# Performance work log

Hardware: AMD Instinct MI355X
Metric: run time of the kernel (lower is better)

The kernel has to match this reference:

```python
import jax, jax.numpy as jnp
import numpy as np

H = 16  # num_heads
B, N, M, D = 4, 512, 2048, 1024
FF = 4096  # mlp_ratio * D
LN_EPS = 1e-5


def _ln(x, g, b):
    m = x.mean(-1, keepdims=True)
    v = ((x - m) ** 2).mean(-1, keepdims=True)
    return (x - m) * jax.lax.rsqrt(v + LN_EPS) * g + b


def _attn(q_in, k_in, v_in, wq, bq, wk, bk, wv, bv, wp, bp):
    b, n, d = q_in.shape
    m = k_in.shape[1]
    hd = d // H
    scale = hd ** -0.5
    q = (q_in @ wq + bq).reshape(b, n, H, hd) * scale
    k = (k_in @ wk + bk).reshape(b, m, H, hd)
    v = (v_in @ wv + bv).reshape(b, m, H, hd)
    attn = jax.nn.softmax(jnp.einsum('bnhd,bmhd->bhnm', q, k), axis=-1)
    out = jnp.einsum('bhnm,bmhd->bnhd', attn, v).reshape(b, n, d)
    return out @ wp + bp


def setup_inputs() -> dict:
    key = jax.random.key(0)
    ks = iter(jax.random.split(key, 32))
    rnd = lambda shape: jax.random.normal(next(ks), shape, dtype=jnp.float32)
    w = lambda *shape: rnd(shape) * 0.02
    inp = {
        'state': rnd((B, N, D)),
        'patches': rnd((B, M, D)),
        'patches_pos_embed': rnd((B, M, D)),
        'state_query': rnd((B, N, D)),
    }
    for p in ('ca', 'sa'):
        inp[f'{p}_wq'] = w(D, D); inp[f'{p}_bq'] = jnp.zeros((D,), jnp.float32)
        inp[f'{p}_wk'] = w(D, D); inp[f'{p}_bk'] = jnp.zeros((D,), jnp.float32)
        inp[f'{p}_wv'] = w(D, D); inp[f'{p}_bv'] = jnp.zeros((D,), jnp.float32)
        inp[f'{p}_wp'] = w(D, D); inp[f'{p}_bp'] = jnp.zeros((D,), jnp.float32)
    inp['w1'] = w(D, FF); inp['b1'] = jnp.zeros((FF,), jnp.float32)
    inp['w2'] = w(FF, D); inp['b2'] = jnp.zeros((D,), jnp.float32)
    for i in (1, 2, 3):
        inp[f'n{i}_g'] = jnp.ones((D,), jnp.float32)
        inp[f'n{i}_b'] = jnp.zeros((D,), jnp.float32)
        inp[f'ls{i}'] = jnp.full((D,), 1e-5, jnp.float32)
    return inp


def reference(state, patches, patches_pos_embed, state_query,
              ca_wq, ca_bq, ca_wk, ca_bk, ca_wv, ca_bv, ca_wp, ca_bp,
              sa_wq, sa_bq, sa_wk, sa_bk, sa_wv, sa_bv, sa_wp, sa_bp,
              w1, b1, w2, b2,
              n1_g, n1_b, n2_g, n2_b, n3_g, n3_b,
              ls1, ls2, ls3):
    # pre-norm path of TransformerLayer.forward_pre (dropouts/drop_path = 0)
    state = state + state_query
    kv = patches + patches_pos_embed
    cross = _attn(_ln(state, n1_g, n1_b), kv, patches,
                  ca_wq, ca_bq, ca_wk, ca_bk, ca_wv, ca_bv, ca_wp, ca_bp)
    state = state + cross * ls1
    ns = _ln(state, n2_g, n2_b)
    selfa = _attn(ns, ns, ns,
                  sa_wq, sa_bq, sa_wk, sa_bk, sa_wv, sa_bv, sa_wp, sa_bp)
    state = state + selfa * ls2
    h = jax.nn.gelu(_ln(state, n3_g, n3_b) @ w1 + b1)
    return state + (h @ w2 + b2) * ls3
```

## Files before the change

### kernel.cpp

```cpp
#include <hip/hip_runtime.h>

#define DEV __device__ __forceinline__

typedef __bf16 bf16x8 __attribute__((ext_vector_type(8)));
typedef float f32x4 __attribute__((ext_vector_type(4)));

DEV unsigned short f2bf(float f) {
  __bf16 h = (__bf16)f;
  return __builtin_bit_cast(unsigned short, h);
}
DEV unsigned int cvtpk(float lo, float hi) {
  unsigned int r;
  asm("v_cvt_pk_bf16_f32 %0, %1, %2" : "=v"(r) : "v"(lo), "v"(hi));
  return r;
}

DEV void gload16(const void* g, void* l) {
  __builtin_amdgcn_global_load_lds(
      (const __attribute__((address_space(1))) unsigned int*)g,
      (__attribute__((address_space(3))) unsigned int*)l, 16, 0, 0);
}

DEV void tconv64_body(const float* __restrict__ W, unsigned short* __restrict__ Wt,
                      int K, int N, int bx, int by, float* tile ) {
  const int t = threadIdx.x;
  const int rr = t >> 4;
  const int cc = (t & 15) * 4;
#pragma unroll
  for (int it = 0; it < 4; it++) {
    float4 v = *reinterpret_cast<const float4*>(
        &W[(size_t)(by * 64 + it * 16 + rr) * N + bx * 64 + cc]);
    tile[(it * 16 + rr) * 65 + cc] = v.x;
    tile[(it * 16 + rr) * 65 + cc + 1] = v.y;
    tile[(it * 16 + rr) * 65 + cc + 2] = v.z;
    tile[(it * 16 + rr) * 65 + cc + 3] = v.w;
  }
  __syncthreads();
  const int nr = t >> 3;
  const int kc = (t & 7) * 8;
#pragma unroll
  for (int it = 0; it < 2; it++) {
    const int n = it * 32 + nr;
    uint4 o;
    o.x = cvtpk(tile[(kc + 0) * 65 + n], tile[(kc + 1) * 65 + n]);
    o.y = cvtpk(tile[(kc + 2) * 65 + n], tile[(kc + 3) * 65 + n]);
    o.z = cvtpk(tile[(kc + 4) * 65 + n], tile[(kc + 5) * 65 + n]);
    o.w = cvtpk(tile[(kc + 6) * 65 + n], tile[(kc + 7) * 65 + n]);
    *reinterpret_cast<uint4*>(&Wt[(size_t)(bx * 64 + n) * K + by * 64 + kc]) = o;
  }
}

DEV void add_ln_body(const float* __restrict__ a, const float* b, float* x0_out,
                     unsigned short* __restrict__ y, const float* __restrict__ gam,
                     const float* __restrict__ bet, int row) {
  const int t = threadIdx.x;
  const int c = t * 4;
  const size_t base = (size_t)row * 1024 + c;
  float4 v = *reinterpret_cast<const float4*>(a + base);
  if (b) {
    float4 v2 = *reinterpret_cast<const float4*>(b + base);
    v.x += v2.x; v.y += v2.y; v.z += v2.z; v.w += v2.w;
  }
  if (x0_out) *reinterpret_cast<float4*>(x0_out + base) = v;
  float s = v.x + v.y + v.z + v.w;
  float sq = v.x * v.x + v.y * v.y + v.z * v.z + v.w * v.w;
#pragma unroll
  for (int o = 32; o > 0; o >>= 1) {
    s += __shfl_xor(s, o);
    sq += __shfl_xor(sq, o);
  }
  __shared__ float ps[4], pq[4];
  const int w = t >> 6;
  if ((t & 63) == 0) { ps[w] = s; pq[w] = sq; }
  __syncthreads();
  s = ps[0] + ps[1] + ps[2] + ps[3];
  sq = pq[0] + pq[1] + pq[2] + pq[3];
  const float mean = s * (1.f / 1024.f);
  const float var = sq * (1.f / 1024.f) - mean * mean;
  const float rstd = rsqrtf(var + 1e-5f);
  float4 gv = *reinterpret_cast<const float4*>(gam + c);
  float4 bv = *reinterpret_cast<const float4*>(bet + c);
  uint2 o2;
  o2.x = cvtpk((v.x - mean) * rstd * gv.x + bv.x, (v.y - mean) * rstd * gv.y + bv.y);
  o2.y = cvtpk((v.z - mean) * rstd * gv.z + bv.z, (v.w - mean) * rstd * gv.w + bv.w);
  *reinterpret_cast<uint2*>(y + base) = o2;
}

DEV void kvcast_body8(const float* __restrict__ p, const float* __restrict__ pe,
                      unsigned short* __restrict__ kvo, unsigned short* __restrict__ po,
                      int bid) {
  const size_t i = ((size_t)bid * 256 + threadIdx.x) * 8;
  float4 a0 = *reinterpret_cast<const float4*>(p + i);
  float4 a1 = *reinterpret_cast<const float4*>(p + i + 4);
  float4 b0 = *reinterpret_cast<const float4*>(pe + i);
  float4 b1 = *reinterpret_cast<const float4*>(pe + i + 4);
  uint4 kv, pp;
  kv.x = cvtpk(a0.x + b0.x, a0.y + b0.y);
  kv.y = cvtpk(a0.z + b0.z, a0.w + b0.w);
  kv.z = cvtpk(a1.x + b1.x, a1.y + b1.y);
  kv.w = cvtpk(a1.z + b1.z, a1.w + b1.w);
  pp.x = cvtpk(a0.x, a0.y);
  pp.y = cvtpk(a0.z, a0.w);
  pp.z = cvtpk(a1.x, a1.y);
  pp.w = cvtpk(a1.z, a1.w);
  *reinterpret_cast<uint4*>(kvo + i) = kv;
  *reinterpret_cast<uint4*>(po + i) = pp;
}

struct Pre {
  const float* caw[3]; unsigned short* cad[3];
  const float* state; const float* squery; float* stateF; unsigned short* lnB;
  const float* n1_g; const float* n1_b;
  const float* patches; const float* ppe; unsigned short* kvB; unsigned short* patB;
};
__global__ __launch_bounds__(256) void prelude_kernel(Pre p) {
  __shared__ __align__(16) float tile[64 * 65];
  const int bid = blockIdx.x;
  if (bid < 4096) {
    kvcast_body8(p.patches, p.ppe, p.kvB, p.patB, bid);
  } else if (bid < 4864) {
    const int i = bid - 4096;
    const int m = i >> 8, wi = i & 255;
    tconv64_body(p.caw[m], p.cad[m], 1024, 1024, wi & 15, wi >> 4, tile);
  } else {
    add_ln_body(p.state, p.squery, p.stateF, p.lnB, p.n1_g, p.n1_b, bid - 4864);
  }
}

__global__ __launch_bounds__(256) void add_ln_kernel(
    const float* __restrict__ a, const float* b, float* x0_out,
    unsigned short* __restrict__ y, const float* __restrict__ gam,
    const float* __restrict__ bet) {
  add_ln_body(a, b, x0_out, y, gam, bet, blockIdx.x);
}

DEV void xcd_swizzle(int gx, int gy, int& bx, int& by, int& bz) {
  const int gxy = gx * gy;
  const int nwg = gxy * gridDim.z;
  const int orig = (blockIdx.z * gy + blockIdx.y) * gx + blockIdx.x;
  const int q = nwg >> 3, r = nwg & 7;
  const int xcd = orig & 7;
  int wgid = (xcd < r ? xcd * (q + 1) : r * (q + 1) + (xcd - r) * q) + (orig >> 3);
  bz = wgid / gxy;
  wgid -= bz * gxy;
  if (gy >= gx) { by = wgid / gx; bx = wgid - by * gx; }
  else          { bx = wgid / gy; by = wgid - bx * gy; }
}

template <int BM, int BN>
DEV void gemm_core(const unsigned short* __restrict__ A,
                   const unsigned short* __restrict__ Bt,
                   unsigned short* As, unsigned short* Bs,
                   int brow, int bcol, int K, int lda, int koff,
                   f32x4 (&acc)[BM / 32][BN / 32]) {
  constexpr int WM = BM / 32, WN = BN / 32;
  const int t = threadIdx.x;
  const int lane = t & 63, w = t >> 6;
  const int wr = w >> 1, wc = w & 1;
  const int g = lane >> 4, lr = lane & 15;
  const int srow = lane >> 2, scol = (lane & 3) * 8;

  auto stage = [&](int buf, int k0) {
#pragma unroll
    for (int i = 0; i < BM / 64; i++) {
      const int r0 = (i * 4 + w) * 16;
      gload16(A + (size_t)(brow + r0 + srow) * lda + koff + k0 + scol,
              &As[buf * BM * 32 + r0 * 32]);
    }
#pragma unroll
    for (int i = 0; i < BN / 64; i++) {
      const int r0 = (i * 4 + w) * 16;
      gload16(Bt + (size_t)(bcol + r0 + srow) * lda + koff + k0 + scol,
              &Bs[buf * BN * 32 + r0 * 32]);
    }
  };

  stage(0, 0);
  const int nk = K / 32;
  int cur = 0;
  for (int kt = 0; kt < nk; kt++) {
    __syncthreads();
    if (kt + 1 < nk) stage(cur ^ 1, (kt + 1) * 32);
    bf16x8 af[WM], bfr[WN];
#pragma unroll
    for (int m = 0; m < WM; m++)
      af[m] = *reinterpret_cast<const bf16x8*>(
          &As[cur * BM * 32 + (wr * (BM / 2) + m * 16 + lr) * 32 + g * 8]);
#pragma unroll
    for (int n = 0; n < WN; n++)
      bfr[n] = *reinterpret_cast<const bf16x8*>(
          &Bs[cur * BN * 32 + (wc * (BN / 2) + n * 16 + lr) * 32 + g * 8]);
    __builtin_amdgcn_s_setprio(1);
#pragma unroll
    for (int m = 0; m < WM; m++)
#pragma unroll
      for (int n = 0; n < WN; n++)
        acc[m][n] = __builtin_amdgcn_mfma_f32_16x16x32_bf16(af[m], bfr[n], acc[m][n], 0, 0, 0);
    __builtin_amdgcn_s_setprio(0);
    cur ^= 1;
  }
}

template <int BM, int BN>
DEV void epilogue_vT(f32x4 (&acc)[BM / 32][BN / 32], unsigned short* smem,
                     unsigned short* __restrict__ vT, const float* __restrict__ bias,
                     int brow, int bcol, int vcol0, int vNk, int rpb) {
  constexpr int WM = BM / 32, WN = BN / 32;
  constexpr int LDT = 136;
  const int t = threadIdx.x, lane = t & 63, w = t >> 6;
  const int wr = w >> 1, wc = w & 1;
  const int g = lane >> 4, lr = lane & 15;
  __syncthreads();
#pragma unroll
  for (int m = 0; m < WM; m++) {
    const int row0 = wr * (BM / 2) + m * 16 + g * 4;
#pragma unroll
    for (int n = 0; n < WN; n++) {
      const int cc = wc * (BN / 2) + n * 16 + lr;
      const float bv = bias[bcol + cc];
      uint2 pk;
      pk.x = cvtpk(acc[m][n][0] + bv, acc[m][n][1] + bv);
      pk.y = cvtpk(acc[m][n][2] + bv, acc[m][n][3] + bv);
      *reinterpret_cast<uint2*>(&smem[cc * LDT + row0]) = pk;
    }
  }
  __syncthreads();
  const int b = brow / rpb;
  const int kvb = brow % rpb;
  constexpr int ITERS = BM * BN / (256 * 8);
#pragma unroll
  for (int it = 0; it < ITERS; it++) {
    const int idx = it * 256 + t;
    const int cc = idx / (BM / 8);
    const int ch = idx % (BM / 8);
    const int dg = bcol + cc - vcol0;
    const int h = dg >> 6, d = dg & 63;
    uint4 v = *reinterpret_cast<uint4*>(&smem[cc * LDT + ch * 8]);
    *reinterpret_cast<uint4*>(
        &vT[((size_t)(b * 16 + h) * 64 + d) * vNk + kvb + ch * 8]) = v;
  }
}

template <int EPI, int BM, int BN>
__global__ __launch_bounds__(256) void gemm_kernel(
    const unsigned short* __restrict__ A, const unsigned short* __restrict__ Bt,
    const float* __restrict__ bias, const float* resid,
    const float* __restrict__ ls, void* outp, int M, int N, int K, int lda,
    unsigned short* vT, int vcol0, int vNk, int rpb) {
  constexpr int WM = BM / 32;
  constexpr int WN = BN / 32;
  constexpr int STG = 2 * BM * 32 + 2 * BN * 32;
  constexpr int TRN = BN * 136;
  constexpr int SME = (EPI == 5 && TRN > STG) ? TRN : STG;
  __shared__ __align__(16) unsigned short smem[SME];
  unsigned short* As = smem;
  unsigned short* Bs = smem + 2 * BM * 32;
  const int t = threadIdx.x;
  const int lane = t & 63, w = t >> 6;
  const int wr = w >> 1, wc = w & 1;
  const int g = lane >> 4, lr = lane & 15;

  int bx, by, bz;
  xcd_swizzle(gridDim.x, gridDim.y, bx, by, bz);
  const int brow = by * BM, bcol = bx * BN;

  f32x4 acc[WM][WN] = {};
  gemm_core<BM, BN>(A, Bt, As, Bs, brow, bcol, K, lda, bz * K, acc);

  if (EPI == 5 && bcol >= vcol0) {
    epilogue_vT<BM, BN>(acc, smem, vT, bias, brow, bcol, vcol0, vNk, rpb);
    return;
  }

#pragma unroll
  for (int m = 0; m < WM; m++) {
    const int row0 = brow + wr * (BM / 2) + m * 16 + g * 4;
#pragma unroll
    for (int n = 0; n < WN; n++) {
      const int col = bcol + wc * (BN / 2) + n * 16 + lr;
      const float bv = (EPI == 4) ? 0.f : bias[col];
#pragma unroll
      for (int r = 0; r < 4; r++) {
        const float v = acc[m][n][r] + bv;
        const size_t idx = (size_t)(row0 + r) * N + col;
        if (EPI == 0 || EPI == 5) {
          ((unsigned short*)outp)[idx] = f2bf(v);
        } else if (EPI == 2) {
          ((float*)outp)[idx] = resid[idx] + v * ls[col];
        } else if (EPI == 3) {
          const float tth = tanhf(0.7978845608028654f * (v + 0.044715f * v * v * v));
          ((unsigned short*)outp)[idx] = f2bf(0.5f * v * (1.f + tth));
        } else {
          ((float*)outp)[(size_t)bz * M * N + idx] = v;
        }
      }
    }
  }
}

struct G3X {
  const unsigned short* A[3]; const unsigned short* Bt[3];
  const float* bias[3]; unsigned short* out[3]; int ecum[3];
  unsigned short* vT; int vNk; int rpb;
  const float* wp; unsigned short* wpt;
  const float* saw[4]; unsigned short* sad[4];
  const float* w1; unsigned short* w1t;
  const float* w2; unsigned short* w2t;
  const float* bq; const float* bk; const float* bv; float* bqkv;
};
__global__ __launch_bounds__(256) void gemm3_kernel(G3X p, int N, int K) {
  constexpr int BM = 128, BN = 128, WM = BM / 32, WN = BN / 32;
  constexpr int STG = 2 * BM * 32 + 2 * BN * 32;
  constexpr int TRN = BN * 136;
  constexpr int SME = (TRN > STG) ? TRN : STG;
  constexpr int NG = 1152;
  __shared__ __align__(16) unsigned short smem[SME];
  const int bid = blockIdx.x;
  const int t = threadIdx.x;

  if (bid >= NG) {
    float* tile = reinterpret_cast<float*>(smem);
    int i = bid - NG;
    if (i < 256) {
      tconv64_body(p.wp, p.wpt, 1024, 1024, i & 15, i >> 4, tile);
    } else if (i < 1280) {
      i -= 256;
      const int m = i >> 8, wi = i & 255;
      tconv64_body(p.saw[m], p.sad[m], 1024, 1024, wi & 15, wi >> 4, tile);
    } else if (i < 2304) {
      i -= 1280;
      tconv64_body(p.w1, p.w1t, 1024, 4096, i & 63, i >> 6, tile);
    } else if (i < 3328) {
      i -= 2304;
      tconv64_body(p.w2, p.w2t, 4096, 1024, i & 15, i >> 4, tile);
    } else {
      const int j = (i - 3328) * 256 + t;
      p.bqkv[j] = j < 1024 ? p.bq[j] : (j < 2048 ? p.bk[j - 1024] : p.bv[j - 2048]);
    }
    return;
  }

  unsigned short* As = smem;
  unsigned short* Bs = smem + 2 * BM * 32;
  const int lane = t & 63, w = t >> 6;
  const int wr = w >> 1, wc = w & 1;
  const int g = lane >> 4, lr = lane & 15;
  const int wgid = (bid & 7) * (NG >> 3) + (bid >> 3);
  const int by = wgid >> 3, bx = wgid & 7;
  const int s = (by >= p.ecum[0]) + (by >= p.ecum[1]);
  const int byloc = by - (s ? p.ecum[s - 1] : 0);
  const unsigned short* A = p.A[s];
  const unsigned short* Bt = p.Bt[s];
  const float* bias = p.bias[s];
  const int brow = byloc * BM, bcol = bx * BN;

  f32x4 acc[WM][WN] = {};
  gemm_core<BM, BN>(A, Bt, As, Bs, brow, bcol, K, K, 0, acc);

  if (s == 2) {
    epilogue_vT<BM, BN>(acc, smem, p.vT, bias, brow, bcol, 0, p.vNk, p.rpb);
    return;
  }
  unsigned short* outp = p.out[s];
#pragma unroll
  for (int m = 0; m < WM; m++) {
    const int row0 = brow + wr * (BM / 2) + m * 16 + g * 4;
#pragma unroll
    for (int n = 0; n < WN; n++) {
      const int col = bcol + wc * (BN / 2) + n * 16 + lr;
      const float bv = bias[col];
#pragma unroll
      for (int r = 0; r < 4; r++)
        outp[(size_t)(row0 + r) * N + col] = f2bf(acc[m][n][r] + bv);
    }
  }
}

__global__ __launch_bounds__(256) void splitk_red_kernel(
    const float* __restrict__ p, const float* __restrict__ bias,
    const float* __restrict__ resid, const float* __restrict__ ls,
    float* __restrict__ out) {
  const size_t i = ((size_t)blockIdx.x * 256 + threadIdx.x) * 4;
  const int c = (int)(i & 1023);
  float4 a = *reinterpret_cast<const float4*>(p + i);
  float4 b = *reinterpret_cast<const float4*>(p + 2048ull * 1024 + i);
  float4 rv = *reinterpret_cast<const float4*>(resid + i);
  float4 bb = *reinterpret_cast<const float4*>(bias + c);
  float4 lv = *reinterpret_cast<const float4*>(ls + c);
  float4 o;
  o.x = rv.x + (a.x + b.x + bb.x) * lv.x;
  o.y = rv.y + (a.y + b.y + bb.y) * lv.y;
  o.z = rv.z + (a.z + b.z + bb.z) * lv.z;
  o.w = rv.w + (a.w + b.w + bb.w) * lv.w;
  *reinterpret_cast<float4*>(out + i) = o;
}

__global__ __launch_bounds__(512) void attn_kernel(
    const unsigned short* __restrict__ Q, const unsigned short* __restrict__ Kp,
    const unsigned short* __restrict__ vT, unsigned short* __restrict__ O,
    int RSq, int RSk, int Nq, int Nk, float k2) {
  __shared__ __align__(16) unsigned short Ks[2][128 * 72];
  __shared__ __align__(16) unsigned short Vs[2][64 * 136];
  __shared__ __align__(16) unsigned short Ps[128 * 136];
  const int t = threadIdx.x, lane = t & 63, w = t >> 6;
  const int qt = blockIdx.y, h = blockIdx.x & 15, b = blockIdx.x >> 4;
  const int g = lane >> 4, lr = lane & 15;
  const int ksrow = t >> 2, kscol = (t & 3) * 16;
  const int vsrow = t >> 3, vscol = (t & 7) * 16;

  uint4 qr[2];
  {
    const unsigned short* qp = Q + (size_t)(b * Nq + qt * 128 + w * 16 + lr) * RSq + h * 64 + g * 8;
    qr[0] = *reinterpret_cast<const uint4*>(qp);
    qr[1] = *reinterpret_cast<const uint4*>(qp + 32);
  }
  float m_i = -1e30f, l_i = 0.f;
  f32x4 acc_o[4] = {};

  auto kaddr = [&](int kv0) {
    return reinterpret_cast<const uint4*>(
        Kp + (size_t)(b * Nk + kv0 + ksrow) * RSk + h * 64 + kscol);
  };
  auto vaddr = [&](int kv0) {
    return reinterpret_cast<const uint4*>(
        vT + ((size_t)(b * 16 + h) * 64 + vsrow) * Nk + kv0 + vscol);
  };

  uint4 kr0 = kaddr(0)[0], kr1 = kaddr(0)[1];
  uint4 vr0 = vaddr(0)[0], vr1 = vaddr(0)[1];

  int cur = 0;
  for (int kv0 = 0; kv0 < Nk; kv0 += 128) {
    *reinterpret_cast<uint4*>(&Ks[cur][ksrow * 72 + kscol]) = kr0;
    *reinterpret_cast<uint4*>(&Ks[cur][ksrow * 72 + kscol + 8]) = kr1;
    *reinterpret_cast<uint4*>(&Vs[cur][vsrow * 136 + vscol]) = vr0;
    *reinterpret_cast<uint4*>(&Vs[cur][vsrow * 136 + vscol + 8]) = vr1;
    __syncthreads();
    if (kv0 + 128 < Nk) {
      kr0 = kaddr(kv0 + 128)[0]; kr1 = kaddr(kv0 + 128)[1];
      vr0 = vaddr(kv0 + 128)[0]; vr1 = vaddr(kv0 + 128)[1];
    }

    f32x4 accs[8] = {};
    __builtin_amdgcn_s_setprio(1);
#pragma unroll
    for (int d0 = 0; d0 < 64; d0 += 32) {
      bf16x8 qf = __builtin_bit_cast(bf16x8, qr[d0 >> 5]);
#pragma unroll
      for (int m = 0; m < 8; m++) {
        bf16x8 kf = *reinterpret_cast<const bf16x8*>(&Ks[cur][(m * 16 + lr) * 72 + d0 + g * 8]);
        accs[m] = __builtin_amdgcn_mfma_f32_16x16x32_bf16(kf, qf, accs[m], 0, 0, 0);
      }
    }
    __builtin_amdgcn_s_setprio(0);
    float pmax = -1e30f;
#pragma unroll
    for (int m = 0; m < 8; m++)
#pragma unroll
      for (int r = 0; r < 4; r++) pmax = fmaxf(pmax, accs[m][r]);
    pmax = fmaxf(pmax, __shfl_xor(pmax, 16));
    pmax = fmaxf(pmax, __shfl_xor(pmax, 32));
    const float pm2 = pmax * k2;
    if (!__all(pm2 <= m_i + 8.f)) {
      const float m_new = fmaxf(m_i, pm2);
      const float corr = exp2f(m_i - m_new);
      m_i = m_new;
      l_i *= corr;
#pragma unroll
      for (int r = 0; r < 4; r++) {
        const float cf = __shfl(corr, g * 4 + r);
#pragma unroll
        for (int n = 0; n < 4; n++) acc_o[n][r] *= cf;
      }
    }
    float psum = 0.f;
#pragma unroll
    for (int m = 0; m < 8; m++) {
      float p0 = exp2f(fmaf(accs[m][0], k2, -m_i));
      float p1 = exp2f(fmaf(accs[m][1], k2, -m_i));
      float p2 = exp2f(fmaf(accs[m][2], k2, -m_i));
      float p3 = exp2f(fmaf(accs[m][3], k2, -m_i));
      psum += p0 + p1 + p2 + p3;
      uint2 pk;
      pk.x = cvtpk(p0, p1);
      pk.y = cvtpk(p2, p3);
      *reinterpret_cast<uint2*>(&Ps[(w * 16 + lr) * 136 + m * 16 + g * 4]) = pk;
    }
    psum += __shfl_xor(psum, 16);
    psum += __shfl_xor(psum, 32);
    l_i += psum;
    __builtin_amdgcn_s_setprio(1);
#pragma unroll
    for (int ks = 0; ks < 4; ks++) {
      bf16x8 pf = *reinterpret_cast<const bf16x8*>(&Ps[(w * 16 + lr) * 136 + ks * 32 + g * 8]);
#pragma unroll
      for (int n = 0; n < 4; n++) {
        bf16x8 vf = *reinterpret_cast<const bf16x8*>(&Vs[cur][(n * 16 + lr) * 136 + ks * 32 + g * 8]);
        acc_o[n] = __builtin_amdgcn_mfma_f32_16x16x32_bf16(pf, vf, acc_o[n], 0, 0, 0);
      }
    }
    __builtin_amdgcn_s_setprio(0);
    cur ^= 1;
  }
#pragma unroll
  for (int r = 0; r < 4; r++) {
    const float li = __shfl(l_i, g * 4 + r);
    const float inv = 1.f / li;
    const int qrow = qt * 128 + w * 16 + g * 4 + r;
#pragma unroll
    for (int n = 0; n < 4; n++)
      O[(size_t)(b * Nq + qrow) * 1024 + h * 64 + n * 16 + lr] = f2bf(acc_o[n][r] * inv);
  }
}

extern "C" void kernel_launch(void* const* d_in, const int* in_sizes, int n_in,
                              void* d_out, int out_size, void* d_ws, size_t ws_size,
                              hipStream_t stream) {
  const float* state = (const float*)d_in[0];
  const float* patches = (const float*)d_in[1];
  const float* ppe = (const float*)d_in[2];
  const float* squery = (const float*)d_in[3];
  const float* ca_wq = (const float*)d_in[4];
  const float* ca_bq = (const float*)d_in[5];
  const float* ca_wk = (const float*)d_in[6];
  const float* ca_bk = (const float*)d_in[7];
  const float* ca_wv = (const float*)d_in[8];
  const float* ca_bv = (const float*)d_in[9];
  const float* ca_wp = (const float*)d_in[10];
  const float* ca_bp = (const float*)d_in[11];
  const float* sa_wq = (const float*)d_in[12];
  const float* sa_bq = (const float*)d_in[13];
  const float* sa_wk = (const float*)d_in[14];
  const float* sa_bk = (const float*)d_in[15];
  const float* sa_wv = (const float*)d_in[16];
  const float* sa_bv = (const float*)d_in[17];
  const float* sa_wp = (const float*)d_in[18];
  const float* sa_bp = (const float*)d_in[19];
  const float* w1 = (const float*)d_in[20];
  const float* b1 = (const float*)d_in[21];
  const float* w2 = (const float*)d_in[22];
  const float* b2 = (const float*)d_in[23];
  const float* n1_g = (const float*)d_in[24];
  const float* n1_b = (const float*)d_in[25];
  const float* ls1 = (const float*)d_in[26];
  const float* n2_g = (const float*)d_in[27];
  const float* n2_b = (const float*)d_in[28];
  const float* ls2 = (const float*)d_in[29];
  const float* n3_g = (const float*)d_in[30];
  const float* n3_b = (const float*)d_in[31];
  const float* ls3 = (const float*)d_in[32];

  char* wsp = (char*)d_ws;
  auto alloc = [&](size_t bytes) {
    void* p = (void*)wsp;
    wsp += (bytes + 255) & ~(size_t)255;
    return p;
  };
  float* stateF = (float*)alloc(2048ull * 1024 * 4);
  unsigned short* lnB = (unsigned short*)alloc(2048ull * 1024 * 2);
  unsigned short* kvB = (unsigned short*)alloc(8192ull * 1024 * 2);
  unsigned short* patB = (unsigned short*)alloc(8192ull * 1024 * 2);
  unsigned short* qB = (unsigned short*)alloc(2048ull * 1024 * 2);
  unsigned short* kB = (unsigned short*)alloc(8192ull * 1024 * 2);
  unsigned short* vB = (unsigned short*)alloc(8192ull * 1024 * 2);
  unsigned short* oB = (unsigned short*)alloc(2048ull * 1024 * 2);
  unsigned short* hB = kvB;
  unsigned short* qkvB = kB;
  unsigned short* vTc = vB;
  unsigned short* vTs = qB;
  float* mlp2p = (float*)patB;
  unsigned short* ca_wqt = (unsigned short*)alloc(1024ull * 1024 * 2);
  unsigned short* ca_wkt = (unsigned short*)alloc(1024ull * 1024 * 2);
  unsigned short* ca_wvt = (unsigned short*)alloc(1024ull * 1024 * 2);
  unsigned short* ca_wpt = (unsigned short*)alloc(1024ull * 1024 * 2);
  unsigned short* sa_wqkvt = (unsigned short*)alloc(3072ull * 1024 * 2);
  unsigned short* sa_wpt = (unsigned short*)alloc(1024ull * 1024 * 2);
  unsigned short* w1t = (unsigned short*)alloc(4096ull * 1024 * 2);
  unsigned short* w2t = (unsigned short*)alloc(4096ull * 1024 * 2);
  float* sa_bqkv = (float*)alloc(3072 * 4);

  Pre pre;
  pre.caw[0] = ca_wq; pre.cad[0] = ca_wqt;
  pre.caw[1] = ca_wk; pre.cad[1] = ca_wkt;
  pre.caw[2] = ca_wv; pre.cad[2] = ca_wvt;
  pre.state = state; pre.squery = squery; pre.stateF = stateF; pre.lnB = lnB;
  pre.n1_g = n1_g; pre.n1_b = n1_b;
  pre.patches = patches; pre.ppe = ppe; pre.kvB = kvB; pre.patB = patB;
  prelude_kernel<<<6912, 256, 0, stream>>>(pre);

  const float k2 = 0.125f * 1.4426950408889634f;

  G3X g3;
  g3.A[0] = lnB;  g3.Bt[0] = ca_wqt; g3.bias[0] = ca_bq; g3.out[0] = qB;      g3.ecum[0] = 16;
  g3.A[1] = kvB;  g3.Bt[1] = ca_wkt; g3.bias[1] = ca_bk; g3.out[1] = kB;      g3.ecum[1] = 80;
  g3.A[2] = patB; g3.Bt[2] = ca_wvt; g3.bias[2] = ca_bv; g3.out[2] = nullptr; g3.ecum[2] = 144;
  g3.vT = vTc; g3.vNk = 2048; g3.rpb = 2048;
  g3.wp = ca_wp; g3.wpt = ca_wpt;
  g3.saw[0] = sa_wq; g3.sad[0] = sa_wqkvt;
  g3.saw[1] = sa_wk; g3.sad[1] = sa_wqkvt + 1024ull * 1024;
  g3.saw[2] = sa_wv; g3.sad[2] = sa_wqkvt + 2048ull * 1024;
  g3.saw[3] = sa_wp; g3.sad[3] = sa_wpt;
  g3.w1 = w1; g3.w1t = w1t; g3.w2 = w2; g3.w2t = w2t;
  g3.bq = sa_bq; g3.bk = sa_bk; g3.bv = sa_bv; g3.bqkv = sa_bqkv;
  gemm3_kernel<<<4492, 256, 0, stream>>>(g3, 1024, 1024);
  attn_kernel<<<dim3(64, 4), 512, 0, stream>>>(qB, kB, vTc, oB, 1024, 1024, 512, 2048, k2);
  gemm_kernel<2, 64, 64><<<dim3(16, 32), 256, 0, stream>>>(oB, ca_wpt, ca_bp, stateF, ls1, stateF, 2048, 1024, 1024, 1024, nullptr, 0, 0, 0);

  add_ln_kernel<<<2048, 256, 0, stream>>>(stateF, nullptr, nullptr, lnB, n2_g, n2_b);
  gemm_kernel<5, 128, 64><<<dim3(48, 16), 256, 0, stream>>>(lnB, sa_wqkvt, sa_bqkv, nullptr, nullptr, qkvB, 2048, 3072, 1024, 1024, vTs, 2048, 512, 512);
  attn_kernel<<<dim3(64, 4), 512, 0, stream>>>(qkvB, qkvB + 1024, vTs, oB, 3072, 3072, 512, 512, k2);
  gemm_kernel<2, 64, 64><<<dim3(16, 32), 256, 0, stream>>>(oB, sa_wpt, sa_bp, stateF, ls2, stateF, 2048, 1024, 1024, 1024, nullptr, 0, 0, 0);

  add_ln_kernel<<<2048, 256, 0, stream>>>(stateF, nullptr, nullptr, lnB, n3_g, n3_b);
  gemm_kernel<3, 128, 128><<<dim3(32, 16), 256, 0, stream>>>(lnB, w1t, b1, nullptr, nullptr, hB, 2048, 4096, 1024, 1024, nullptr, 0, 0, 0);
  gemm_kernel<4, 128, 64><<<dim3(16, 16, 2), 256, 0, stream>>>(hB, w2t, nullptr, nullptr, nullptr, mlp2p, 2048, 1024, 2048, 4096, nullptr, 0, 0, 0);
  splitk_red_kernel<<<2048, 256, 0, stream>>>(mlp2p, b2, stateF, ls3, (float*)d_out);
}
```

Before: 277.0 us.

## Move MLP weight transposes into self-attn QKV GEMM launch; cheaper GELU

The w1/w2 fp32-to-bf16 transpose blocks move out of the first fused GEMM launch and into a new dedicated self-attention QKV GEMM kernel, which appends them as extra tail blocks. This balances work across the two launches so the conversion overlaps with a GEMM that has fewer tiles. The GELU epilogue also replaces tanhf with an exp2-based tanh formula to cut transcendental cost, which may slightly change numerics for large inputs.

After: 277.7 us (median of 2 runs). Within noise of the previous version (+0.3%).

```diff
diff --git a/kernel.cpp b/kernel.cpp
--- a/kernel.cpp
+++ b/kernel.cpp
@@ -19,6 +19,12 @@
   __builtin_amdgcn_global_load_lds(
       (const __attribute__((address_space(1))) unsigned int*)g,
       (__attribute__((address_space(3))) unsigned int*)l, 16, 0, 0);
+}
+
+DEV float gelu(float v) {
+  const float u = 0.7978845608028654f * (v + 0.044715f * v * v * v);
+  const float e = exp2f(u * 2.885390081777927f);
+  return 0.5f * v * (2.f - 2.f / (e + 1.f));
 }
 
 DEV void tconv64_body(const float* __restrict__ W, unsigned short* __restrict__ Wt,
@@ -245,14 +251,10 @@
 __global__ __launch_bounds__(256) void gemm_kernel(
     const unsigned short* __restrict__ A, const unsigned short* __restrict__ Bt,
     const float* __restrict__ bias, const float* resid,
-    const float* __restrict__ ls, void* outp, int M, int N, int K, int lda,
-    unsigned short* vT, int vcol0, int vNk, int rpb) {
+    const float* __restrict__ ls, void* outp, int M, int N, int K, int lda) {
   constexpr int WM = BM / 32;
   constexpr int WN = BN / 32;
-  constexpr int STG = 2 * BM * 32 + 2 * BN * 32;
-  constexpr int TRN = BN * 136;
-  constexpr int SME = (EPI == 5 && TRN > STG) ? TRN : STG;
-  __shared__ __align__(16) unsigned short smem[SME];
+  __shared__ __align__(16) unsigned short smem[2 * BM * 32 + 2 * BN * 32];
   unsigned short* As = smem;
   unsigned short* Bs = smem + 2 * BM * 32;
   const int t = threadIdx.x;
@@ -267,11 +269,6 @@
   f32x4 acc[WM][WN] = {};
   gemm_core<BM, BN>(A, Bt, As, Bs, brow, bcol, K, lda, bz * K, acc);
 
-  if (EPI == 5 && bcol >= vcol0) {
-    epilogue_vT<BM, BN>(acc, smem, vT, bias, brow, bcol, vcol0, vNk, rpb);
-    return;
-  }
-
 #pragma unroll
   for (int m = 0; m < WM; m++) {
     const int row0 = brow + wr * (BM / 2) + m * 16 + g * 4;
@@ -283,13 +280,12 @@
       for (int r = 0; r < 4; r++) {
         const float v = acc[m][n][r] + bv;
         const size_t idx = (size_t)(row0 + r) * N + col;
-        if (EPI == 0 || EPI == 5) {
+        if (EPI == 0) {
           ((unsigned short*)outp)[idx] = f2bf(v);
         } else if (EPI == 2) {
           ((float*)outp)[idx] = resid[idx] + v * ls[col];
         } else if (EPI == 3) {
-          const float tth = tanhf(0.7978845608028654f * (v + 0.044715f * v * v * v));
-          ((unsigned short*)outp)[idx] = f2bf(0.5f * v * (1.f + tth));
+          ((unsigned short*)outp)[idx] = f2bf(gelu(v));
         } else {
           ((float*)outp)[(size_t)bz * M * N + idx] = v;
         }
@@ -304,8 +300,6 @@
   unsigned short* vT; int vNk; int rpb;
   const float* wp; unsigned short* wpt;
   const float* saw[4]; unsigned short* sad[4];
-  const float* w1; unsigned short* w1t;
-  const float* w2; unsigned short* w2t;
   const float* bq; const float* bk; const float* bv; float* bqkv;
 };
 __global__ __launch_bounds__(256) void gemm3_kernel(G3X p, int N, int K) {
@@ -327,14 +321,8 @@
       i -= 256;
       const int m = i >> 8, wi = i & 255;
       tconv64_body(p.saw[m], p.sad[m], 1024, 1024, wi & 15, wi >> 4, tile);
-    } else if (i < 2304) {
-      i -= 1280;
-      tconv64_body(p.w1, p.w1t, 1024, 4096, i & 63, i >> 6, tile);
-    } else if (i < 3328) {
-      i -= 2304;
-      tconv64_body(p.w2, p.w2t, 4096, 1024, i & 15, i >> 4, tile);
     } else {
-      const int j = (i - 3328) * 256 + t;
+      const int j = (i - 1280) * 256 + t;
       p.bqkv[j] = j < 1024 ? p.bq[j] : (j < 2048 ? p.bk[j - 1024] : p.bv[j - 2048]);
     }
     return;
@@ -372,6 +360,63 @@
 #pragma unroll
       for (int r = 0; r < 4; r++)
         outp[(size_t)(row0 + r) * N + col] = f2bf(acc[m][n][r] + bv);
+    }
+  }
+}
+
+struct G5X {
+  const unsigned short* A; const unsigned short* Bt;
+  const float* bias; unsigned short* out;
+  unsigned short* vT; int vcol0; int vNk; int rpb;
+  const float* w1; unsigned short* w1t;
+  const float* w2; unsigned short* w2t;
+};
+__global__ __launch_bounds__(256) void gemm5x_kernel(G5X p, int M, int N, int K) {
+  constexpr int BM = 128, BN = 64, WM = BM / 32, WN = BN / 32;
+  constexpr int STG = 2 * BM * 32 + 2 * BN * 32;
+  __shared__ __align__(16) unsigned short smem[STG];
+  constexpr int NG = 768;
+  const int bid = blockIdx.x;
+  const int t = threadIdx.x;
+
+  if (bid >= NG) {
+    float* tile = reinterpret_cast<float*>(smem);
+    int i = bid - NG;
+    if (i < 1024) {
+      tconv64_body(p.w1, p.w1t, 1024, 4096, i & 63, i >> 6, tile);
+    } else {
+      i -= 1024;
+      tconv64_body(p.w2, p.w2t, 4096, 1024, i & 15, i >> 4, tile);
+    }
+    return;
+  }
+
+  unsigned short* As = smem;
+  unsigned short* Bs = smem + 2 * BM * 32;
+  const int lane = t & 63, w = t >> 6;
+  const int wr = w >> 1, wc = w & 1;
+  const int g = lane >> 4, lr = lane & 15;
+  const int wgid = (bid & 7) * (NG >> 3) + (bid >> 3);
+  const int bx = wgid >> 4, by = wgid & 15;
+  const int brow = by * BM, bcol = bx * BN;
+
+  f32x4 acc[WM][WN] = {};
+  gemm_core<BM, BN>(p.A, p.Bt, As, Bs, brow, bcol, K, K, 0, acc);
+
+  if (bcol >= p.vcol0) {
+    epilogue_vT<BM, BN>(acc, smem, p.vT, p.bias, brow, bcol, p.vcol0, p.vNk, p.rpb);
+    return;
+  }
+#pragma unroll
+  for (int m = 0; m < WM; m++) {
+    const int row0 = brow + wr * (BM / 2) + m * 16 + g * 4;
+#pragma unroll
+    for (int n = 0; n < WN; n++) {
+      const int col = bcol + wc * (BN / 2) + n * 16 + lr;
+      const float bv = p.bias[col];
+#pragma unroll
+      for (int r = 0; r < 4; r++)
+        p.out[(size_t)(row0 + r) * N + col] = f2bf(acc[m][n][r] + bv);
     }
   }
 }
@@ -600,19 +645,22 @@
   g3.saw[1] = sa_wk; g3.sad[1] = sa_wqkvt + 1024ull * 1024;
   g3.saw[2] = sa_wv; g3.sad[2] = sa_wqkvt + 2048ull * 1024;
   g3.saw[3] = sa_wp; g3.sad[3] = sa_wpt;
-  g3.w1 = w1; g3.w1t = w1t; g3.w2 = w2; g3.w2t = w2t;
   g3.bq = sa_bq; g3.bk = sa_bk; g3.bv = sa_bv; g3.bqkv = sa_bqkv;
-  gemm3_kernel<<<4492, 256, 0, stream>>>(g3, 1024, 1024);
+  gemm3_kernel<<<2444, 256, 0, stream>>>(g3, 1024, 1024);
   attn_kernel<<<dim3(64, 4), 512, 0, stream>>>(qB, kB, vTc, oB, 1024, 1024, 512, 2048, k2);
-  gemm_kernel<2, 64, 64><<<dim3(16, 32), 256, 0, stream>>>(oB, ca_wpt, ca_bp, stateF, ls1, stateF, 2048, 1024, 1024, 1024, nullptr, 0, 0, 0);
+  gemm_kernel<2, 64, 64><<<dim3(16, 32), 256, 0, stream>>>(oB, ca_wpt, ca_bp, stateF, ls1, stateF, 2048, 1024, 1024, 1024);
 
   add_ln_kernel<<<2048, 256, 0, stream>>>(stateF, nullptr, nullptr, lnB, n2_g, n2_b);
-  gemm_kernel<5, 128, 64><<<dim3(48, 16), 256, 0, stream>>>(lnB, sa_wqkvt, sa_bqkv, nullptr, nullptr, qkvB, 2048, 3072, 1024, 1024, vTs, 2048, 512, 512);
+  G5X g5;
+  g5.A = lnB; g5.Bt = sa_wqkvt; g5.bias = sa_bqkv; g5.out = qkvB;
+  g5.vT = vTs; g5.vcol0 = 2048; g5.vNk = 512; g5.rpb = 512;
+  g5.w1 = w1; g5.w1t = w1t; g5.w2 = w2; g5.w2t = w2t;
+  gemm5x_kernel<<<2816, 256, 0, stream>>>(g5, 2048, 3072, 1024);
   attn_kernel<<<dim3(64, 4), 512, 0, stream>>>(qkvB, qkvB + 1024, vTs, oB, 3072, 3072, 512, 512, k2);
-  gemm_kernel<2, 64, 64><<<dim3(16, 32), 256, 0, stream>>>(oB, sa_wpt, sa_bp, stateF, ls2, stateF, 2048, 1024, 1024, 1024, nullptr, 0, 0, 0);
+  gemm_kernel<2, 64, 64><<<dim3(16, 32), 256, 0, stream>>>(oB, sa_wpt, sa_bp, stateF, ls2, stateF, 2048, 1024, 1024, 1024);
 
   add_ln_kernel<<<2048, 256, 0, stream>>>(stateF, nullptr, nullptr, lnB, n3_g, n3_b);
-  gemm_kernel<3, 128, 128><<<dim3(32, 16), 256, 0, stream>>>(lnB, w1t, b1, nullptr, nullptr, hB, 2048, 4096, 1024, 1024, nullptr, 0, 0, 0);
-  gemm_kernel<4, 128, 64><<<dim3(16, 16, 2), 256, 0, stream>>>(hB, w2t, nullptr, nullptr, nullptr, mlp2p, 2048, 1024, 2048, 4096, nullptr, 0, 0, 0);
+  gemm_kernel<3, 128, 128><<<dim3(32, 16), 256, 0, stream>>>(lnB, w1t, b1, nullptr, nullptr, hB, 2048, 4096, 1024, 1024);
+  gemm_kernel<4, 128, 64><<<dim3(16, 16, 2), 256, 0, stream>>>(hB, w2t, nullptr, nullptr, nullptr, mlp2p, 2048, 1024, 2048, 4096);
   splitk_red_kernel<<<2048, 256, 0, stream>>>(mlp2p, b2, stateF, ls3, (float*)d_out);
 }
```
